# Optimization experiments

Measured on AMD Instinct MI355X. Metric: run time of the kernel, lower is better.

The kernel has to match this reference:

```python
import jax, jax.numpy as jnp
import numpy as np

B, N1, K, E, H = 64, 8, 128, 256, 512


def setup_inputs() -> dict:
    key = jax.random.key(0)
    ks = jax.random.split(key, 10)
    s = 1.0 / np.sqrt(E)
    sh = 1.0 / np.sqrt(H)
    return {
        "queries": jax.random.normal(ks[0], (B, N1, E), jnp.float32),
        "keys": jax.random.normal(ks[1], (B, N1, K, E), jnp.float32),
        "cum_subs_masks": jax.random.randint(ks[2], (B, N1, K, 1), 0, 2, jnp.int32),
        "num_neg": N1 - 1,
        "wk_w": jax.random.uniform(ks[3], (H, E), jnp.float32, -s, s),
        "wk_b": jax.random.uniform(ks[4], (H,), jnp.float32, -s, s),
        "wq_w": jax.random.uniform(ks[5], (H, E), jnp.float32, -s, s),
        "wq_b": jax.random.uniform(ks[6], (H,), jnp.float32, -s, s),
        "wv_w": jax.random.uniform(ks[7], (1, H), jnp.float32, -sh, sh),
        "wv_b": jax.random.uniform(ks[8], (1,), jnp.float32, -sh, sh),
    }


def reference(queries, keys, cum_subs_masks, num_neg, wk_w, wk_b, wq_w, wq_b, wv_w, wv_b):
    # queries: (B, N1, E) -> project and broadcast over keys dim
    q_proj = jnp.einsum("bne,he->bnh", queries, wq_w) + wq_b        # (B, N1, H)
    k_proj = jnp.einsum("bnke,he->bnkh", keys, wk_w) + wk_b          # (B, N1, K, H)
    hidden = jnp.tanh(q_proj[:, :, None, :] + k_proj)                # (B, N1, K, H)
    scores = jnp.einsum("bnkh,oh->bnko", hidden, wv_w) + wv_b        # (B, N1, K, 1)
    scores = scores + cum_subs_masks.astype(scores.dtype) * (-1e9)
    attn_weight = jax.nn.softmax(scores, axis=-2)                    # over K
    attn_out = jnp.sum(attn_weight * keys, axis=-2)                  # (B, N1, E)
    return attn_out, attn_weight
```

## Files before the change

### kernel.cpp

```cpp
#include <hip/hip_runtime.h>
#include <hip/hip_bf16.h>

#define B_  64
#define N1_ 8
#define KK  128
#define EE  256
#define HH  512
#define BN  (B_ * N1_)

typedef __attribute__((ext_vector_type(8))) short short8;
typedef __attribute__((ext_vector_type(4))) float f32x4;

__device__ __forceinline__ short bfs(float f) {
  __hip_bfloat16 h = __float2bfloat16(f);
  return __builtin_bit_cast(short, h);
}
__device__ __forceinline__ float bf2f(short s) {
  unsigned int u = ((unsigned int)(unsigned short)s) << 16;
  return __builtin_bit_cast(float, u);
}
__device__ __forceinline__ float tanhf_fast(float x) {
  float e2 = __builtin_amdgcn_exp2f(2.8853900817779268f * x);
  return 1.0f - 2.0f * __builtin_amdgcn_rcpf(e2 + 1.0f);
}

__device__ __forceinline__ void gload16(const void* g, void* l) {
  __builtin_amdgcn_global_load_lds(
      (const __attribute__((address_space(1))) void*)g,
      (__attribute__((address_space(3))) void*)l, 16, 0, 0);
}

__global__ __launch_bounds__(256) void k_prep(
    const float* __restrict__ wk_w,
    const float* __restrict__ queries,
    const float* __restrict__ wq_w,
    const float* __restrict__ wq_b,
    const float* __restrict__ wk_b,
    unsigned short* __restrict__ wk_fr,
    float* __restrict__ qp) {
  const int bid = blockIdx.x, t = threadIdx.x;
  if (bid < 64) {
    const int g  = bid * 256 + t;
    const int h  = g >> 5;
    const int e0 = (g & 31) * 8;
    float4 x = *(const float4*)(wk_w + (size_t)h * EE + e0);
    float4 y = *(const float4*)(wk_w + (size_t)h * EE + e0 + 4);
    short8 f;
    f[0] = bfs(x.x); f[1] = bfs(x.y); f[2] = bfs(x.z); f[3] = bfs(x.w);
    f[4] = bfs(y.x); f[5] = bfs(y.y); f[6] = bfs(y.z); f[7] = bfs(y.w);
    const int ht = h >> 4, hl = h & 15;
    const int s = e0 >> 5, lg = (e0 >> 3) & 3;
    const int chunk = (ht * 8 + s) * 64 + lg * 16 + hl;
    *(short8*)(wk_fr + (size_t)chunk * 8) = f;
  } else {
    const int w = t >> 6, l = t & 63, lg = l >> 4, ll = l & 15;
    const int g2 = bid - 64;
    const int bn0 = (g2 >> 1) * 16;
    const int ht0 = (g2 & 1) * 16;
    short8 af[8];
    {
      const float* qr = queries + (size_t)(bn0 + ll) * EE + lg * 8;
      #pragma unroll
      for (int s = 0; s < 8; ++s) {
        float4 x = *(const float4*)(qr + s * 32);
        float4 y = *(const float4*)(qr + s * 32 + 4);
        short8 f;
        f[0] = bfs(x.x); f[1] = bfs(x.y); f[2] = bfs(x.z); f[3] = bfs(x.w);
        f[4] = bfs(y.x); f[5] = bfs(y.y); f[6] = bfs(y.z); f[7] = bfs(y.w);
        af[s] = f;
      }
    }
    #pragma unroll
    for (int i = 0; i < 4; ++i) {
      const int ht = ht0 + w * 4 + i;
      const float* bp = wq_w + (size_t)(ht * 16 + ll) * EE + lg * 8;
      f32x4 a = {0.f, 0.f, 0.f, 0.f};
      #pragma unroll
      for (int s = 0; s < 8; ++s) {
        float4 x = *(const float4*)(bp + s * 32);
        float4 y = *(const float4*)(bp + s * 32 + 4);
        short8 f;
        f[0] = bfs(x.x); f[1] = bfs(x.y); f[2] = bfs(x.z); f[3] = bfs(x.w);
        f[4] = bfs(y.x); f[5] = bfs(y.y); f[6] = bfs(y.z); f[7] = bfs(y.w);
        a = __builtin_amdgcn_mfma_f32_16x16x32_bf16(af[s], f, a, 0, 0, 0);
      }
      const int h = ht * 16 + ll;
      const float add = wq_b[h] + wk_b[h];
      #pragma unroll
      for (int r = 0; r < 4; ++r)
        qp[(size_t)(bn0 + lg * 4 + r) * HH + h] = a[r] + add;
    }
  }
}

__global__ __launch_bounds__(256, 2) void k_fused(
    const float* __restrict__ keys,
    const unsigned short* __restrict__ wk_fr,
    const float* __restrict__ wv_w,
    const float* __restrict__ qp,
    const int* __restrict__ masks,
    float* __restrict__ out) {
  const int t  = threadIdx.x;
  const int w  = t >> 6;
  const int l  = t & 63;
  const int lg = l >> 4;
  const int ll = l & 15;
  const int bn = blockIdx.x;

  __shared__ __align__(16) char bsm[3 * 8192];
  __shared__ float qb_s[HH];
  __shared__ float wv_s[HH];
  __shared__ float sc[KK];
  __shared__ float red[2];
  __shared__ float po[4][256];

  qb_s[t]       = qp[(size_t)bn * HH + t];
  qb_s[t + 256] = qp[(size_t)bn * HH + t + 256];
  wv_s[t]       = wv_w[t];
  wv_s[t + 256] = wv_w[t + 256];

  short8 af0[8], af1[8];
  {
    const float* kp0 = keys + (size_t)(bn * KK + w * 32 + ll) * EE + lg * 8;
    const float* kp1 = kp0 + 16 * EE;
    #pragma unroll
    for (int s = 0; s < 8; ++s) {
      float4 x = *(const float4*)(kp0 + s * 32);
      float4 y = *(const float4*)(kp0 + s * 32 + 4);
      short8 f;
      f[0] = bfs(x.x); f[1] = bfs(x.y); f[2] = bfs(x.z); f[3] = bfs(x.w);
      f[4] = bfs(y.x); f[5] = bfs(y.y); f[6] = bfs(y.z); f[7] = bfs(y.w);
      af0[s] = f;
      x = *(const float4*)(kp1 + s * 32);
      y = *(const float4*)(kp1 + s * 32 + 4);
      f[0] = bfs(x.x); f[1] = bfs(x.y); f[2] = bfs(x.z); f[3] = bfs(x.w);
      f[4] = bfs(y.x); f[5] = bfs(y.y); f[6] = bfs(y.z); f[7] = bfs(y.w);
      af1[s] = f;
    }
  }
  __syncthreads();

  const char* wkb = (const char*)wk_fr;

#define STAGE(ti, off) {                                                     \
    const char* s_ = wkb + (size_t)(ti) * 8192 + (size_t)t * 16;             \
    char* d_ = bsm + (off) + w * 1024;                                       \
    gload16(s_, d_);                                                         \
    gload16(s_ + 4096, d_ + 4096); }

  STAGE(0, 0);
  STAGE(1, 8192);

  float p0[4] = {0.f, 0.f, 0.f, 0.f};
  float p1[4] = {0.f, 0.f, 0.f, 0.f};
  int off0 = 0, off1 = 8192, off2 = 16384;

#define COMPUTE(roff, ii) {                                                  \
    f32x4 a0 = {0.f, 0.f, 0.f, 0.f};                                         \
    f32x4 a1 = {0.f, 0.f, 0.f, 0.f};                                         \
    __builtin_amdgcn_s_setprio(1);                                           \
    _Pragma("unroll") for (int s = 0; s < 8; ++s) {                          \
      short8 bfr = *(const short8*)(bsm + (roff) + s * 1024 + l * 16);       \
      a0 = __builtin_amdgcn_mfma_f32_16x16x32_bf16(af0[s], bfr, a0, 0, 0, 0);\
      a1 = __builtin_amdgcn_mfma_f32_16x16x32_bf16(af1[s], bfr, a1, 0, 0, 0);\
    }                                                                        \
    __builtin_amdgcn_s_setprio(0);                                           \
    const int h = (ii) * 16 + ll;                                            \
    const float qb = qb_s[h];                                                \
    const float wv = wv_s[h];                                                \
    _Pragma("unroll") for (int r = 0; r < 4; ++r) {                          \
      p0[r] += wv * tanhf_fast(a0[r] + qb);                                  \
      p1[r] += wv * tanhf_fast(a1[r] + qb); } }

  #pragma unroll 1
  for (int i = 0; i < 30; ++i) {
    asm volatile("s_waitcnt vmcnt(2)" ::: "memory");
    __builtin_amdgcn_s_barrier();
    __builtin_amdgcn_sched_barrier(0);
    STAGE(i + 2, off2);
    COMPUTE(off0, i);
    int tmp = off0; off0 = off1; off1 = off2; off2 = tmp;
  }
  asm volatile("s_waitcnt vmcnt(2)" ::: "memory");
  __builtin_amdgcn_s_barrier();
  __builtin_amdgcn_sched_barrier(0);
  COMPUTE(off0, 30);
  { int tmp = off0; off0 = off1; off1 = off2; off2 = tmp; }
  asm volatile("s_waitcnt vmcnt(0)" ::: "memory");
  __builtin_amdgcn_s_barrier();
  __builtin_amdgcn_sched_barrier(0);
  COMPUTE(off0, 31);
#undef COMPUTE
#undef STAGE

  #pragma unroll
  for (int r = 0; r < 4; ++r) {
    #pragma unroll
    for (int off = 1; off <= 8; off <<= 1) {
      p0[r] += __shfl_xor(p0[r], off, 64);
      p1[r] += __shfl_xor(p1[r], off, 64);
    }
  }
  if (ll == 0) {
    #pragma unroll
    for (int r = 0; r < 4; ++r) {
      sc[w * 32 + lg * 4 + r]      = p0[r];
      sc[w * 32 + 16 + lg * 4 + r] = p1[r];
    }
  }
  __syncthreads();

  if (t < KK) sc[t] += (float)masks[bn * KK + t] * (-1e9f);
  __syncthreads();
  if (t < 64) {
    float a = fmaxf(sc[t], sc[t + 64]);
    #pragma unroll
    for (int off = 32; off >= 1; off >>= 1) a = fmaxf(a, __shfl_xor(a, off, 64));
    if (t == 0) red[0] = a;
  }
  __syncthreads();
  const float m = red[0];
  if (t < KK) sc[t] = expf(sc[t] - m);
  __syncthreads();
  if (t < 64) {
    float a = sc[t] + sc[t + 64];
    #pragma unroll
    for (int off = 32; off >= 1; off >>= 1) a += __shfl_xor(a, off, 64);
    if (t == 0) red[1] = a;
  }
  __syncthreads();
  const float inv = 1.f / red[1];
  if (t < KK) {
    float wgt = sc[t] * inv;
    sc[t] = wgt;
    out[BN * EE + (size_t)bn * KK + t] = wgt;
  }
  __syncthreads();

  {
    const float wgt0 = sc[w * 32 + ll];
    const float wgt1 = sc[w * 32 + 16 + ll];
    #pragma unroll
    for (int s = 0; s < 8; ++s) {
      float pv[8];
      #pragma unroll
      for (int j = 0; j < 8; ++j)
        pv[j] = wgt0 * bf2f(af0[s][j]) + wgt1 * bf2f(af1[s][j]);
      #pragma unroll
      for (int j = 0; j < 8; ++j) {
        #pragma unroll
        for (int off = 1; off <= 8; off <<= 1)
          pv[j] += __shfl_xor(pv[j], off, 64);
      }
      if (ll == 0) {
        float4 v0 = {pv[0], pv[1], pv[2], pv[3]};
        float4 v1 = {pv[4], pv[5], pv[6], pv[7]};
        *(float4*)(&po[w][lg * 8 + s * 32])     = v0;
        *(float4*)(&po[w][lg * 8 + s * 32 + 4]) = v1;
      }
    }
  }
  __syncthreads();
  out[(size_t)bn * EE + t] = po[0][t] + po[1][t] + po[2][t] + po[3][t];
}

extern "C" void kernel_launch(void* const* d_in, const int* in_sizes, int n_in,
                              void* d_out, int out_size, void* d_ws, size_t ws_size,
                              hipStream_t stream) {
  const float* queries = (const float*)d_in[0];
  const float* keys    = (const float*)d_in[1];
  const int*   masks   = (const int*)d_in[2];
  const float* wk_w = (const float*)d_in[4];
  const float* wk_b = (const float*)d_in[5];
  const float* wq_w = (const float*)d_in[6];
  const float* wq_b = (const float*)d_in[7];
  const float* wv_w = (const float*)d_in[8];

  float* out = (float*)d_out;
  float* qp  = (float*)d_ws;
  unsigned short* wk_fr = (unsigned short*)(qp + BN * HH);

  k_prep<<<128, 256, 0, stream>>>(wk_w, queries, wq_w, wq_b, wk_b, wk_fr, qp);
  k_fused<<<BN, 256, 0, stream>>>(keys, wk_fr, wv_w, qp, masks, out);
}
```

Baseline: 55.76 us.

## Load Wk fragments directly into registers, double-buffered, instead of via LDS

Replaces the LDS-staged triple-buffered global_load_lds pipeline for Wk B-fragments with per-wave direct global_load_dwordx4 into two register sets (A/B), ping-ponged with vmcnt waits and no block barriers. It also packs the q-projection and wv into one float2 LDS array so one LDS read serves both. The aim is to remove LDS traffic and workgroup-wide barriers in the main loop. In exchange every wave fetches the weight tiles itself, raising global/L2 traffic, and 64 extra VGPRs may cut occupancy.

```diff
diff --git a/kernel.cpp b/kernel.cpp
--- a/kernel.cpp
+++ b/kernel.cpp
@@ -22,12 +22,6 @@
 __device__ __forceinline__ float tanhf_fast(float x) {
   float e2 = __builtin_amdgcn_exp2f(2.8853900817779268f * x);
   return 1.0f - 2.0f * __builtin_amdgcn_rcpf(e2 + 1.0f);
-}
-
-__device__ __forceinline__ void gload16(const void* g, void* l) {
-  __builtin_amdgcn_global_load_lds(
-      (const __attribute__((address_space(1))) void*)g,
-      (__attribute__((address_space(3))) void*)l, 16, 0, 0);
 }
 
 __global__ __launch_bounds__(256) void k_prep(
@@ -107,17 +101,17 @@
   const int ll = l & 15;
   const int bn = blockIdx.x;
 
-  __shared__ __align__(16) char bsm[3 * 8192];
-  __shared__ float qb_s[HH];
-  __shared__ float wv_s[HH];
+  __shared__ float2 qw_s[HH];
   __shared__ float sc[KK];
   __shared__ float red[2];
   __shared__ float po[4][256];
 
-  qb_s[t]       = qp[(size_t)bn * HH + t];
-  qb_s[t + 256] = qp[(size_t)bn * HH + t + 256];
-  wv_s[t]       = wv_w[t];
-  wv_s[t + 256] = wv_w[t + 256];
+  {
+    float2 v0; v0.x = qp[(size_t)bn * HH + t];       v0.y = wv_w[t];
+    float2 v1; v1.x = qp[(size_t)bn * HH + t + 256]; v1.y = wv_w[t + 256];
+    qw_s[t] = v0;
+    qw_s[t + 256] = v1;
+  }
 
   short8 af0[8], af1[8];
   {
@@ -141,57 +135,86 @@
   __syncthreads();
 
   const char* wkb = (const char*)wk_fr;
-
-#define STAGE(ti, off) {                                                     \
-    const char* s_ = wkb + (size_t)(ti) * 8192 + (size_t)t * 16;             \
-    char* d_ = bsm + (off) + w * 1024;                                       \
-    gload16(s_, d_);                                                         \
-    gload16(s_ + 4096, d_ + 4096); }
-
-  STAGE(0, 0);
-  STAGE(1, 8192);
+  const int lofs = l * 16;
 
   float p0[4] = {0.f, 0.f, 0.f, 0.f};
   float p1[4] = {0.f, 0.f, 0.f, 0.f};
-  int off0 = 0, off1 = 8192, off2 = 16384;
-
-#define COMPUTE(roff, ii) {                                                  \
-    f32x4 a0 = {0.f, 0.f, 0.f, 0.f};                                         \
-    f32x4 a1 = {0.f, 0.f, 0.f, 0.f};                                         \
-    __builtin_amdgcn_s_setprio(1);                                           \
-    _Pragma("unroll") for (int s = 0; s < 8; ++s) {                          \
-      short8 bfr = *(const short8*)(bsm + (roff) + s * 1024 + l * 16);       \
-      a0 = __builtin_amdgcn_mfma_f32_16x16x32_bf16(af0[s], bfr, a0, 0, 0, 0);\
-      a1 = __builtin_amdgcn_mfma_f32_16x16x32_bf16(af1[s], bfr, a1, 0, 0, 0);\
-    }                                                                        \
-    __builtin_amdgcn_s_setprio(0);                                           \
-    const int h = (ii) * 16 + ll;                                            \
-    const float qb = qb_s[h];                                                \
-    const float wv = wv_s[h];                                                \
-    _Pragma("unroll") for (int r = 0; r < 4; ++r) {                          \
-      p0[r] += wv * tanhf_fast(a0[r] + qb);                                  \
-      p1[r] += wv * tanhf_fast(a1[r] + qb); } }
-
+  float4 A0, A1, A2, A3, A4, A5, A6, A7;
+  float4 B0, B1, B2, B3, B4, B5, B6, B7;
+
+#define ISSUE(b0,b1,b2,b3,b4,b5,b6,b7, ti) {                               \
+    const char* p_ = wkb + (size_t)(ti) * 8192 + lofs;                     \
+    const char* q_ = p_ + 4096;                                            \
+    asm volatile(                                                          \
+      "global_load_dwordx4 %0, %8, off\n\t"                                \
+      "global_load_dwordx4 %1, %8, off offset:1024\n\t"                    \
+      "global_load_dwordx4 %2, %8, off offset:2048\n\t"                    \
+      "global_load_dwordx4 %3, %8, off offset:3072\n\t"                    \
+      "global_load_dwordx4 %4, %9, off\n\t"                                \
+      "global_load_dwordx4 %5, %9, off offset:1024\n\t"                    \
+      "global_load_dwordx4 %6, %9, off offset:2048\n\t"                    \
+      "global_load_dwordx4 %7, %9, off offset:3072"                        \
+      : "=&v"(b0), "=&v"(b1), "=&v"(b2), "=&v"(b3),                        \
+        "=&v"(b4), "=&v"(b5), "=&v"(b6), "=&v"(b7)                        \
+      : "v"(p_), "v"(q_)); }
+
+#define WAITV(n)  {                                                        \
+    asm volatile("s_waitcnt vmcnt(" #n ")" ::: "memory");                  \
+    __builtin_amdgcn_sched_barrier(0); }
+
+#define COMPUTE(b0,b1,b2,b3,b4,b5,b6,b7, ii) {                             \
+    f32x4 a0 = {0.f, 0.f, 0.f, 0.f};                                       \
+    f32x4 a1 = {0.f, 0.f, 0.f, 0.f};                                       \
+    short8 f_;                                                             \
+    __builtin_amdgcn_s_setprio(1);                                         \
+    f_ = __builtin_bit_cast(short8, b0);                                   \
+    a0 = __builtin_amdgcn_mfma_f32_16x16x32_bf16(af0[0], f_, a0, 0, 0, 0); \
+    a1 = __builtin_amdgcn_mfma_f32_16x16x32_bf16(af1[0], f_, a1, 0, 0, 0); \
+    f_ = __builtin_bit_cast(short8, b1);                                   \
+    a0 = __builtin_amdgcn_mfma_f32_16x16x32_bf16(af0[1], f_, a0, 0, 0, 0); \
+    a1 = __builtin_amdgcn_mfma_f32_16x16x32_bf16(af1[1], f_, a1, 0, 0, 0); \
+    f_ = __builtin_bit_cast(short8, b2);                                   \
+    a0 = __builtin_amdgcn_mfma_f32_16x16x32_bf16(af0[2], f_, a0, 0, 0, 0); \
+    a1 = __builtin_amdgcn_mfma_f32_16x16x32_bf16(af1[2], f_, a1, 0, 0, 0); \
+    f_ = __builtin_bit_cast(short8, b3);                                   \
+    a0 = __builtin_amdgcn_mfma_f32_16x16x32_bf16(af0[3], f_, a0, 0, 0, 0); \
+    a1 = __builtin_amdgcn_mfma_f32_16x16x32_bf16(af1[3], f_, a1, 0, 0, 0); \
+    f_ = __builtin_bit_cast(short8, b4);                                   \
+    a0 = __builtin_amdgcn_mfma_f32_16x16x32_bf16(af0[4], f_, a0, 0, 0, 0); \
+    a1 = __builtin_amdgcn_mfma_f32_16x16x32_bf16(af1[4], f_, a1, 0, 0, 0); \
+    f_ = __builtin_bit_cast(short8, b5);                                   \
+    a0 = __builtin_amdgcn_mfma_f32_16x16x32_bf16(af0[5], f_, a0, 0, 0, 0); \
+    a1 = __builtin_amdgcn_mfma_f32_16x16x32_bf16(af1[5], f_, a1, 0, 0, 0); \
+    f_ = __builtin_bit_cast(short8, b6);                                   \
+    a0 = __builtin_amdgcn_mfma_f32_16x16x32_bf16(af0[6], f_, a0, 0, 0, 0); \
+    a1 = __builtin_amdgcn_mfma_f32_16x16x32_bf16(af1[6], f_, a1, 0, 0, 0); \
+    f_ = __builtin_bit_cast(short8, b7);                                   \
+    a0 = __builtin_amdgcn_mfma_f32_16x16x32_bf16(af0[7], f_, a0, 0, 0, 0); \
+    a1 = __builtin_amdgcn_mfma_f32_16x16x32_bf16(af1[7], f_, a1, 0, 0, 0); \
+    __builtin_amdgcn_s_setprio(0);                                         \
+    const float2 qw = qw_s[(ii) * 16 + ll];                                \
+    _Pragma("unroll") for (int r = 0; r < 4; ++r) {                        \
+      p0[r] += qw.y * tanhf_fast(a0[r] + qw.x);                            \
+      p1[r] += qw.y * tanhf_fast(a1[r] + qw.x); } }
+
+  ISSUE(A0,A1,A2,A3,A4,A5,A6,A7, 0);
+  ISSUE(B0,B1,B2,B3,B4,B5,B6,B7, 1);
   #pragma unroll 1
-  for (int i = 0; i < 30; ++i) {
-    asm volatile("s_waitcnt vmcnt(2)" ::: "memory");
-    __builtin_amdgcn_s_barrier();
-    __builtin_amdgcn_sched_barrier(0);
-    STAGE(i + 2, off2);
-    COMPUTE(off0, i);
-    int tmp = off0; off0 = off1; off1 = off2; off2 = tmp;
-  }
-  asm volatile("s_waitcnt vmcnt(2)" ::: "memory");
-  __builtin_amdgcn_s_barrier();
-  __builtin_amdgcn_sched_barrier(0);
-  COMPUTE(off0, 30);
-  { int tmp = off0; off0 = off1; off1 = off2; off2 = tmp; }
-  asm volatile("s_waitcnt vmcnt(0)" ::: "memory");
-  __builtin_amdgcn_s_barrier();
-  __builtin_amdgcn_sched_barrier(0);
-  COMPUTE(off0, 31);
+  for (int i = 0; i < 30; i += 2) {
+    WAITV(8);
+    COMPUTE(A0,A1,A2,A3,A4,A5,A6,A7, i);
+    ISSUE(A0,A1,A2,A3,A4,A5,A6,A7, i + 2);
+    WAITV(8);
+    COMPUTE(B0,B1,B2,B3,B4,B5,B6,B7, i + 1);
+    ISSUE(B0,B1,B2,B3,B4,B5,B6,B7, i + 3);
+  }
+  WAITV(8);
+  COMPUTE(A0,A1,A2,A3,A4,A5,A6,A7, 30);
+  WAITV(0);
+  COMPUTE(B0,B1,B2,B3,B4,B5,B6,B7, 31);
 #undef COMPUTE
-#undef STAGE
+#undef WAITV
+#undef ISSUE
 
   #pragma unroll
   for (int r = 0; r < 4; ++r) {
```

Result: faster. 49.81 us (median of 2 runs) (-10.7%).
